# Kernel tuning notes

Hardware: AMD Instinct MI355X
Metric: run time of the kernel (lower is better)

The kernel has to match this reference:

```python
import jax, jax.numpy as jnp
import numpy as np

N, E, F_IN, HID, EDIM = 20000, 320000, 16, 64, 1


def _add_self_loops(src, dst, eattr, n):
    # PyG add_self_loops with fill_value='mean': self-loop edge_attr = mean of
    # incoming edge_attr per destination node (0 if no incoming edges).
    deg = jax.ops.segment_sum(jnp.ones_like(eattr[:, 0]), dst, num_segments=n)
    mean_attr = jax.ops.segment_sum(eattr, dst, num_segments=n) / jnp.maximum(deg, 1.0)[:, None]
    loop = jnp.arange(n)
    return (jnp.concatenate([src, loop]), jnp.concatenate([dst, loop]),
            jnp.concatenate([eattr, mean_attr], axis=0))


def _gat_layer(x, src, dst, eattr, W, a_src, a_dst, We, a_e, b, heads, out_ch, n):
    # shared linear for src/dst (PyG GATConv with int in_channels)
    h = (x @ W).reshape(n, heads, out_ch)                      # [N,H,C]
    al_s = jnp.einsum('nhc,hc->nh', h, a_src)                  # [N,H]
    al_d = jnp.einsum('nhc,hc->nh', h, a_dst)
    ef = (eattr @ We).reshape(-1, heads, out_ch)               # [E,H,C]
    al_e = jnp.einsum('ehc,hc->eh', ef, a_e)                   # [E,H]
    alpha = jax.nn.leaky_relu(al_s[src] + al_d[dst] + al_e, 0.2)
    # segment softmax over destination node
    m = jax.ops.segment_max(alpha, dst, num_segments=n)
    m = jnp.where(jnp.isfinite(m), m, 0.0)
    ex = jnp.exp(alpha - m[dst])
    den = jax.ops.segment_sum(ex, dst, num_segments=n)
    coef = ex / (den[dst] + 1e-16)                             # [E,H]
    out = jax.ops.segment_sum(h[src] * coef[:, :, None], dst, num_segments=n)
    return out.reshape(n, heads * out_ch) + b


def setup_inputs() -> dict:
    key = jax.random.key(0)
    ks = jax.random.split(key, 24)
    s = 0.1
    inp = {
        'x': jax.random.normal(ks[0], (N, F_IN), jnp.float32),
        'edge_index': jax.random.randint(ks[1], (2, E), 0, N, jnp.int64),
        'edge_attr': jax.random.uniform(ks[2], (E, EDIM), jnp.float32),
        # layer 0: heads=4, in=16, out=64
        'W0': jax.random.normal(ks[3], (F_IN, 4 * HID), jnp.float32) * s,
        'as0': jax.random.normal(ks[4], (4, HID), jnp.float32) * s,
        'ad0': jax.random.normal(ks[5], (4, HID), jnp.float32) * s,
        'We0': jax.random.normal(ks[6], (EDIM, 4 * HID), jnp.float32) * s,
        'ae0': jax.random.normal(ks[7], (4, HID), jnp.float32) * s,
        'b0': jnp.zeros((4 * HID,), jnp.float32),
        # layer 1: heads=4, in=256, out=64
        'W1': jax.random.normal(ks[8], (4 * HID, 4 * HID), jnp.float32) * s,
        'as1': jax.random.normal(ks[9], (4, HID), jnp.float32) * s,
        'ad1': jax.random.normal(ks[10], (4, HID), jnp.float32) * s,
        'We1': jax.random.normal(ks[11], (EDIM, 4 * HID), jnp.float32) * s,
        'ae1': jax.random.normal(ks[12], (4, HID), jnp.float32) * s,
        'b1': jnp.zeros((4 * HID,), jnp.float32),
        # layer 2: heads=1, in=256, out=64
        'W2': jax.random.normal(ks[13], (4 * HID, HID), jnp.float32) * s,
        'as2': jax.random.normal(ks[14], (1, HID), jnp.float32) * s,
        'ad2': jax.random.normal(ks[15], (1, HID), jnp.float32) * s,
        'We2': jax.random.normal(ks[16], (EDIM, HID), jnp.float32) * s,
        'ae2': jax.random.normal(ks[17], (1, HID), jnp.float32) * s,
        'b2': jnp.zeros((HID,), jnp.float32),
        'ln_g': jnp.ones((HID,), jnp.float32),
        'ln_b': jnp.zeros((HID,), jnp.float32),
    }
    return inp


def reference(x, edge_index, edge_attr,
              W0, as0, ad0, We0, ae0, b0,
              W1, as1, ad1, We1, ae1, b1,
              W2, as2, ad2, We2, ae2, b2,
              ln_g, ln_b):
    n = x.shape[0]
    src, dst, eattr = _add_self_loops(edge_index[0], edge_index[1], edge_attr, n)
    h = _gat_layer(x, src, dst, eattr, W0, as0, ad0, We0, ae0, b0, 4, HID, n)
    h = jax.nn.elu(h)  # dropout is identity in eval
    h = _gat_layer(h, src, dst, eattr, W1, as1, ad1, We1, ae1, b1, 4, HID, n)
    h = jax.nn.elu(h)
    h = _gat_layer(h, src, dst, eattr, W2, as2, ad2, We2, ae2, b2, 1, HID, n)
    mu = jnp.mean(h, axis=-1, keepdims=True)
    var = jnp.mean((h - mu) ** 2, axis=-1, keepdims=True)
    return (h - mu) / jnp.sqrt(var + 1e-5) * ln_g + ln_b
```

## Files before the change

### kernel.cpp

```cpp
#include <hip/hip_runtime.h>
#include <hip/hip_bf16.h>
#include <math.h>


typedef __attribute__((ext_vector_type(8))) short short8;
typedef __attribute__((ext_vector_type(4))) float float4v;

#define CAP 64

__device__ __forceinline__ float wave_sum(float v) {
#pragma unroll
  for (int off = 32; off > 0; off >>= 1) v += __shfl_xor(v, off, 64);
  return v;
}

__device__ __forceinline__ unsigned short f2bf(float v) {
  unsigned u = __float_as_uint(v);
  unsigned r = u + 0x7fff + ((u >> 16) & 1);
  return (unsigned short)(r >> 16);
}

__device__ __forceinline__ float bf2f(unsigned short u) {
  return __uint_as_float(((unsigned)u) << 16);
}

__device__ __forceinline__ float sel4(float a, float b, float c, float d, int i) {
  return (i == 0) ? a : (i == 1) ? b : (i == 2) ? c : d;
}

__global__ __launch_bounds__(256) void k1_kernel(
    const float* __restrict__ x, const int* __restrict__ srcv, const int* __restrict__ dstv,
    const float* __restrict__ eattr,
    const float* __restrict__ W0, const float* __restrict__ as0, const float* __restrict__ ad0,
    const float* __restrict__ We0, const float* __restrict__ ae0,
    const float* __restrict__ W1, const float* __restrict__ as1, const float* __restrict__ ad1,
    const float* __restrict__ We1, const float* __restrict__ ae1,
    const float* __restrict__ W2, const float* __restrict__ as2, const float* __restrict__ ad2,
    const float* __restrict__ We2, const float* __restrict__ ae2,
    unsigned short* __restrict__ Wf1, unsigned short* __restrict__ Wf2,
    float* __restrict__ wedot, float* __restrict__ al0s, float* __restrict__ al0d,
    int* __restrict__ deg, int2* __restrict__ ebuf,
    int N, int E, int gD) {
  int b = blockIdx.x;
  int tid = threadIdx.x;
  if (b < 272) {
    int idx = b * 256 + tid;
    int j = idx & 7, lane = (idx >> 3) & 63, ks = (idx >> 9) & 7, nt = idx >> 12;
    int k = ks * 32 + (lane >> 4) * 8 + j;
    int col = lane & 15;
    float v = 0.f;
    if (nt < 16) {
      v = W1[(size_t)k * 256 + nt * 16 + col];
    } else if (col < 4) {
      for (int c = 0; c < 64; c++) v = fmaf(W1[(size_t)k * 256 + col * 64 + c], as1[col * 64 + c], v);
    } else if (col < 8) {
      int h = col - 4;
      for (int c = 0; c < 64; c++) v = fmaf(W1[(size_t)k * 256 + h * 64 + c], ad1[h * 64 + c], v);
    }
    Wf1[idx] = f2bf(v);
  } else if (b < 352) {
    int idx = (b - 272) * 256 + tid;
    int j = idx & 7, lane = (idx >> 3) & 63, ks = (idx >> 9) & 7, nt = idx >> 12;
    int k = ks * 32 + (lane >> 4) * 8 + j;
    int col = lane & 15;
    float v = 0.f;
    if (nt < 4) {
      v = W2[(size_t)k * 64 + nt * 16 + col];
    } else if (col < 1) {
      for (int c = 0; c < 64; c++) v = fmaf(W2[(size_t)k * 64 + c], as2[c], v);
    } else if (col < 2) {
      for (int c = 0; c < 64; c++) v = fmaf(W2[(size_t)k * 64 + c], ad2[c], v);
    }
    Wf2[idx] = f2bf(v);
  } else if (b == 352) {
    if (tid >= 64) return;
    int c = tid;
    for (int h = 0; h < 4; h++) {
      float v = wave_sum(We0[h * 64 + c] * ae0[h * 64 + c]);
      if (c == 0) wedot[h] = v;
    }
    for (int h = 0; h < 4; h++) {
      float v = wave_sum(We1[h * 64 + c] * ae1[h * 64 + c]);
      if (c == 0) wedot[4 + h] = v;
    }
    float v = wave_sum(We2[c] * ae2[c]);
    if (c == 0) wedot[8] = v;
  } else if (b < 353 + gD) {
    __shared__ float va[128];
    if (tid < 128) {
      int k = tid >> 3, col = tid & 7;
      float v = 0.f;
      if (col < 4) {
        for (int c = 0; c < 64; c++) v = fmaf(W0[(size_t)k * 256 + col * 64 + c], as0[col * 64 + c], v);
      } else {
        int h = col - 4;
        for (int c = 0; c < 64; c++) v = fmaf(W0[(size_t)k * 256 + h * 64 + c], ad0[h * 64 + c], v);
      }
      va[tid] = v;
    }
    __syncthreads();
    int node = (b - 353) * 256 + tid;
    if (node >= N) return;
    const float4* xr = (const float4*)(x + (size_t)node * 16);
    float4 xv[4];
#pragma unroll
    for (int q = 0; q < 4; q++) xv[q] = xr[q];
    float al[8];
#pragma unroll
    for (int j = 0; j < 8; j++) al[j] = 0.f;
#pragma unroll
    for (int k = 0; k < 16; k++) {
      float xk = ((const float*)xv)[k];
#pragma unroll
      for (int j = 0; j < 8; j++) al[j] = fmaf(xk, va[k * 8 + j], al[j]);
    }
    ((float4*)al0s)[node] = make_float4(al[0], al[1], al[2], al[3]);
    ((float4*)al0d)[node] = make_float4(al[4], al[5], al[6], al[7]);
  } else {
    int e = (b - 353 - gD) * 256 + tid;
    if (e >= E) return;
    int d = dstv[e];
    int s = srcv[e];
    float ea = eattr[e];
    int pos = atomicAdd(&deg[d], 1);
    if (pos < CAP) ebuf[(size_t)d * CAP + pos] = make_int2(s, __float_as_int(ea));
  }
}

__global__ __launch_bounds__(1024) void fused0_kernel(
    const int* __restrict__ deg, const int2* __restrict__ ebuf,
    const float* __restrict__ al0s, const float* __restrict__ al0d,
    const float* __restrict__ wedot,
    const float* __restrict__ x, const float* __restrict__ W0,
    const float* __restrict__ b0, const unsigned short* __restrict__ Wf1,
    unsigned short* __restrict__ buf256, float* __restrict__ al1s,
    float* __restrict__ al1d, int n) {
  __shared__ unsigned short hrow[16][264];
  __shared__ float w0lds[4096];
  int tile = blockIdx.x;
  int wv = threadIdx.x >> 6;
  int lane = threadIdx.x & 63;
  int es = lane >> 4;
  int c = lane & 15;
  int le = lane >> 2;
  int lh = lane & 3;

  ((float4*)w0lds)[threadIdx.x] = ((const float4*)W0)[threadIdx.x];
  __syncthreads();

  int r = wv;
  int node = tile * 16 + r;
  if (node < n) {
    int dg = deg[node];
    int cnt = dg < CAP ? dg : CAP;
    float xself = x[(size_t)node * 16 + c];
    float4 as4s = ((const float4*)al0s)[node];
    float4 ald4 = ((const float4*)al0d)[node];
    float aldP = sel4(ald4.x, ald4.y, ald4.z, ald4.w, lh);
    float wd0 = wedot[0], wd1 = wedot[1], wd2 = wedot[2], wd3 = wedot[3];
    float wdP = sel4(wd0, wd1, wd2, wd3, lh);

    float Z[4] = {0.f, 0.f, 0.f, 0.f};
    float denP = 0.f;
    float easumP = 0.f;

    for (int i = 0; i < cnt; i += 16) {
      int slot = i + le;
      bool av = slot < cnt;
      int2 re = ebuf[(size_t)node * CAP + slot];
      int srcE = av ? re.x : 0;
      float ev = av ? __int_as_float(re.y) : 0.f;
      int srcK[4];
      float xvK[4];
#pragma unroll
      for (int k = 0; k < 4; k++) srcK[k] = __shfl(srcE, (k * 4 + es) * 4, 64);
#pragma unroll
      for (int k = 0; k < 4; k++) xvK[k] = x[(size_t)srcK[k] * 16 + c];
      float a = al0s[(size_t)srcE * 4 + lh] + aldP + ev * wdP;
      a = fmaxf(a, 0.2f * a);
      a = fminf(a, 30.f);
      float wE = av ? __expf(a) : 0.f;
      denP += wE;
      easumP += (lh == 0) ? ev : 0.f;
#pragma unroll
      for (int k = 0; k < 4; k++) {
        int e4 = (k * 4 + es) * 4;
        float w0v = __shfl(wE, e4 + 0, 64);
        float w1v = __shfl(wE, e4 + 1, 64);
        float w2v = __shfl(wE, e4 + 2, 64);
        float w3v = __shfl(wE, e4 + 3, 64);
        Z[0] = fmaf(w0v, xvK[k], Z[0]);
        Z[1] = fmaf(w1v, xvK[k], Z[1]);
        Z[2] = fmaf(w2v, xvK[k], Z[2]);
        Z[3] = fmaf(w3v, xvK[k], Z[3]);
      }
    }

#pragma unroll
    for (int h = 0; h < 4; h++) {
      Z[h] += __shfl_xor(Z[h], 16, 64);
      Z[h] += __shfl_xor(Z[h], 32, 64);
    }
    denP += __shfl_xor(denP, 4, 64);
    denP += __shfl_xor(denP, 8, 64);
    denP += __shfl_xor(denP, 16, 64);
    denP += __shfl_xor(denP, 32, 64);
    float easum = wave_sum(easumP);

    float dsel = __shfl(denP, es, 64);
    float evs = easum / fmaxf((float)dg, 1.f);
    float as_e = sel4(as4s.x, as4s.y, as4s.z, as4s.w, es);
    float ald_e = sel4(ald4.x, ald4.y, ald4.z, ald4.w, es);
    float wd_e = sel4(wd0, wd1, wd2, wd3, es);
    float aS = as_e + ald_e + evs * wd_e;
    aS = fmaxf(aS, 0.2f * aS);
    aS = fminf(aS, 30.f);
    float wvs = __expf(aS);
    dsel += wvs;
    float zsel = sel4(Z[0], Z[1], Z[2], Z[3], es) + wvs * xself;
    float zn = zsel / (dsel + 1e-16f);

    float zc[16];
    int basel = lane & 48;
#pragma unroll
    for (int cc = 0; cc < 16; cc++) zc[cc] = __shfl(zn, basel + cc, 64);
    float o[4];
    float4 b4 = ((const float4*)b0)[lane];
#pragma unroll
    for (int jj = 0; jj < 4; jj++) o[jj] = ((const float*)&b4)[jj];
#pragma unroll
    for (int cc = 0; cc < 16; cc++) {
      float4 w0r = *(const float4*)&w0lds[cc * 256 + lane * 4];
#pragma unroll
      for (int jj = 0; jj < 4; jj++) o[jj] = fmaf(zc[cc], ((const float*)&w0r)[jj], o[jj]);
    }
    ushort4 o4;
    float ox = o[0] > 0.f ? o[0] : expm1f(o[0]);
    float oy = o[1] > 0.f ? o[1] : expm1f(o[1]);
    float oz = o[2] > 0.f ? o[2] : expm1f(o[2]);
    float ow = o[3] > 0.f ? o[3] : expm1f(o[3]);
    o4.x = f2bf(ox);
    o4.y = f2bf(oy);
    o4.z = f2bf(oz);
    o4.w = f2bf(ow);
    *(ushort4*)&hrow[r][lane * 4] = o4;
  } else {
    *(ushort4*)&hrow[r][lane * 4] = make_ushort4(0, 0, 0, 0);
  }
  __syncthreads();

  int m = lane & 15, q = lane >> 4;
  int row0 = tile * 16;
  short8 afrag[8];
#pragma unroll
  for (int ks = 0; ks < 8; ks++) afrag[ks] = *(short8*)&hrow[m][ks * 32 + q * 8];

  const short8* wf = (const short8*)Wf1;
  for (int nt = wv; nt < 17; nt += 16) {
    const short8* bl = wf + (size_t)nt * 8 * 64 + lane;
    short8 bf[8];
#pragma unroll
    for (int ks = 0; ks < 8; ks++) bf[ks] = bl[ks * 64];
    float4v acc = {0.f, 0.f, 0.f, 0.f};
#pragma unroll
    for (int ks = 0; ks < 8; ks++)
      acc = __builtin_amdgcn_mfma_f32_16x16x32_bf16(afrag[ks], bf[ks], acc, 0, 0, 0);
    if (nt < 16) {
      int col = nt * 16 + m;
#pragma unroll
      for (int reg = 0; reg < 4; reg++) {
        int rr = row0 + q * 4 + reg;
        if (rr < n) buf256[(size_t)rr * 256 + col] = f2bf(acc[reg]);
      }
    } else {
#pragma unroll
      for (int reg = 0; reg < 4; reg++) {
        int rr = row0 + q * 4 + reg;
        if (rr < n) {
          if (m < 4) al1s[(size_t)rr * 4 + m] = acc[reg];
          else if (m < 8) al1d[(size_t)rr * 4 + (m - 4)] = acc[reg];
        }
      }
    }
  }
}

__global__ __launch_bounds__(1024) void fused1_kernel(
    const int* __restrict__ deg, const int2* __restrict__ ebuf,
    const float* __restrict__ al1s, const float* __restrict__ al1d,
    const float* __restrict__ wedot,
    const unsigned short* __restrict__ buf256, const float* __restrict__ b1,
    const unsigned short* __restrict__ Wf2, unsigned short* __restrict__ buf64,
    float* __restrict__ al2s, float* __restrict__ al2d, int n) {
  __shared__ unsigned short hrow[16][264];
  int tile = blockIdx.x;
  int wv = threadIdx.x >> 6;
  int lane = threadIdx.x & 63;
  int half = lane >> 5;
  int l = lane & 31;
  int h4 = l >> 3;
  int le = lane >> 2;
  int lh = lane & 3;
  int eA0 = half ? 1 : 0;
  int eB0 = half ? 3 : 2;

  int r = wv;
  int node = tile * 16 + r;
  if (node < n) {
    int dg = deg[node];
    int cnt = dg < CAP ? dg : CAP;
    float aldh = al1d[(size_t)node * 4 + h4];
    float alsh = al1s[(size_t)node * 4 + h4];
    float wdh = wedot[4 + h4];
    float aldP = al1d[(size_t)node * 4 + lh];
    float wdP = wedot[4 + lh];
    short8 rowS = ((const short8*)(buf256 + (size_t)node * 256))[l];

    float acc[8];
#pragma unroll
    for (int j = 0; j < 8; j++) acc[j] = 0.f;
    float denP = 0.f;
    float easumP = 0.f;

    for (int i = 0; i < cnt; i += 16) {
      int slot = i + le;
      bool av = slot < cnt;
      int2 re = ebuf[(size_t)node * CAP + slot];
      int srcE = av ? re.x : 0;
      float ev = av ? __int_as_float(re.y) : 0.f;
      int srcA[4], srcB[4];
#pragma unroll
      for (int k = 0; k < 4; k++) {
        srcA[k] = __shfl(srcE, (k * 4 + eA0) * 4, 64);
        srcB[k] = __shfl(srcE, (k * 4 + eB0) * 4, 64);
      }
      short8 rowA[4], rowB[4];
#pragma unroll
      for (int k = 0; k < 4; k++) {
        rowA[k] = ((const short8*)(buf256 + (size_t)srcA[k] * 256))[l];
        rowB[k] = ((const short8*)(buf256 + (size_t)srcB[k] * 256))[l];
      }
      float a = al1s[(size_t)srcE * 4 + lh] + aldP + ev * wdP;
      a = fmaxf(a, 0.2f * a);
      a = fminf(a, 30.f);
      float wE = av ? __expf(a) : 0.f;
      denP += wE;
      easumP += (lh == 0) ? ev : 0.f;
#pragma unroll
      for (int k = 0; k < 4; k++) {
        float wA = __shfl(wE, (k * 4 + eA0) * 4 + h4, 64);
        float wB = __shfl(wE, (k * 4 + eB0) * 4 + h4, 64);
        const unsigned short* pa = (const unsigned short*)&rowA[k];
        const unsigned short* pb = (const unsigned short*)&rowB[k];
#pragma unroll
        for (int j = 0; j < 8; j++) acc[j] = fmaf(wA, bf2f(pa[j]), acc[j]);
#pragma unroll
        for (int j = 0; j < 8; j++) acc[j] = fmaf(wB, bf2f(pb[j]), acc[j]);
      }
    }

#pragma unroll
    for (int j = 0; j < 8; j++) acc[j] += __shfl_xor(acc[j], 32, 64);
    denP += __shfl_xor(denP, 4, 64);
    denP += __shfl_xor(denP, 8, 64);
    denP += __shfl_xor(denP, 16, 64);
    denP += __shfl_xor(denP, 32, 64);
    float easum = wave_sum(easumP);
    float den = __shfl(denP, h4, 64);

    {
      float evs = easum / fmaxf((float)dg, 1.f);
      float a = alsh + aldh + evs * wdh;
      a = fmaxf(a, 0.2f * a);
      a = fminf(a, 30.f);
      float wvv = __expf(a);
      const unsigned short* ps = (const unsigned short*)&rowS;
      den += wvv;
#pragma unroll
      for (int j = 0; j < 8; j++) acc[j] = fmaf(wvv, bf2f(ps[j]), acc[j]);
    }

    if (half == 0) {
      float inv = 1.f / (den + 1e-16f);
      float4 bb0 = ((const float4*)b1)[l * 2];
      float4 bb1 = ((const float4*)b1)[l * 2 + 1];
      unsigned short o8[8];
#pragma unroll
      for (int j = 0; j < 8; j++) {
        float bjv = (j < 4) ? ((const float*)&bb0)[j] : ((const float*)&bb1)[j - 4];
        float o = acc[j] * inv + bjv;
        o = o > 0.f ? o : expm1f(o);
        o8[j] = f2bf(o);
      }
      *(short8*)&hrow[r][l * 8] = *(short8*)o8;
    }
  } else if (half == 0) {
    unsigned short z8[8] = {0, 0, 0, 0, 0, 0, 0, 0};
    *(short8*)&hrow[r][l * 8] = *(short8*)z8;
  }
  __syncthreads();

  int m = lane & 15, q = lane >> 4;
  int row0 = tile * 16;
  short8 afrag[8];
#pragma unroll
  for (int ks = 0; ks < 8; ks++) afrag[ks] = *(short8*)&hrow[m][ks * 32 + q * 8];

  const short8* wf = (const short8*)Wf2;
  for (int nt = wv; nt < 5; nt += 16) {
    const short8* bl = wf + (size_t)nt * 8 * 64 + lane;
    short8 bf[8];
#pragma unroll
    for (int ks = 0; ks < 8; ks++) bf[ks] = bl[ks * 64];
    float4v acc = {0.f, 0.f, 0.f, 0.f};
#pragma unroll
    for (int ks = 0; ks < 8; ks++)
      acc = __builtin_amdgcn_mfma_f32_16x16x32_bf16(afrag[ks], bf[ks], acc, 0, 0, 0);
    if (nt < 4) {
      int col = nt * 16 + m;
#pragma unroll
      for (int reg = 0; reg < 4; reg++) {
        int rr = row0 + q * 4 + reg;
        if (rr < n) buf64[(size_t)rr * 64 + col] = f2bf(acc[reg]);
      }
    } else {
#pragma unroll
      for (int reg = 0; reg < 4; reg++) {
        int rr = row0 + q * 4 + reg;
        if (rr < n) {
          if (m < 1) al2s[rr] = acc[reg];
          else if (m < 2) al2d[rr] = acc[reg];
        }
      }
    }
  }
}

__global__ __launch_bounds__(256) void agg_ln_kernel(
    const int* __restrict__ deg, const int2* __restrict__ ebuf,
    const float* __restrict__ al2s, const float* __restrict__ al2d,
    const float* __restrict__ wedot,
    const unsigned short* __restrict__ B, const float* __restrict__ bias,
    const float* __restrict__ ln_g, const float* __restrict__ ln_b,
    float* __restrict__ out, int n) {
  int wv = threadIdx.x >> 6;
  int node = blockIdx.x * 4 + wv;
  if (node >= n) return;
  int lane = threadIdx.x & 63;
  int q = lane >> 4;
  int l = lane & 15;
  int le = lane & 15;
  int dg = deg[node];
  int cnt = dg < CAP ? dg : CAP;
  float ald = al2d[node];
  float als = al2s[node];
  float wd = wedot[0];
  ushort4 bvS = ((const ushort4*)(B + (size_t)node * 64))[l];

  float4 acc = make_float4(0.f, 0.f, 0.f, 0.f);
  float denP = 0.f;
  float easumP = 0.f;

  for (int i = 0; i < cnt; i += 16) {
    int slot = i + le;
    bool av = slot < cnt;
    int2 re = ebuf[(size_t)node * CAP + slot];
    int srcE = av ? re.x : 0;
    float ev = av ? __int_as_float(re.y) : 0.f;
    int srcK[4];
#pragma unroll
    for (int k = 0; k < 4; k++) srcK[k] = __shfl(srcE, k * 4 + q, 64);
    ushort4 bvK[4];
#pragma unroll
    for (int k = 0; k < 4; k++) bvK[k] = ((const ushort4*)(B + (size_t)srcK[k] * 64))[l];
    float a = al2s[srcE] + ald + ev * wd;
    a = fmaxf(a, 0.2f * a);
    a = fminf(a, 30.f);
    float wE = av ? __expf(a) : 0.f;
    denP += wE;
    easumP += ev;
#pragma unroll
    for (int k = 0; k < 4; k++) {
      float w = __shfl(wE, k * 4 + q, 64);
      acc.x = fmaf(w, bf2f(bvK[k].x), acc.x);
      acc.y = fmaf(w, bf2f(bvK[k].y), acc.y);
      acc.z = fmaf(w, bf2f(bvK[k].z), acc.z);
      acc.w = fmaf(w, bf2f(bvK[k].w), acc.w);
    }
  }

  acc.x += __shfl_xor(acc.x, 32, 64);
  acc.y += __shfl_xor(acc.y, 32, 64);
  acc.z += __shfl_xor(acc.z, 32, 64);
  acc.w += __shfl_xor(acc.w, 32, 64);
  acc.x += __shfl_xor(acc.x, 16, 64);
  acc.y += __shfl_xor(acc.y, 16, 64);
  acc.z += __shfl_xor(acc.z, 16, 64);
  acc.w += __shfl_xor(acc.w, 16, 64);
  float den = wave_sum(denP) * 0.25f;
  float easum = wave_sum(easumP) * 0.25f;

  {
    float evs = easum / fmaxf((float)dg, 1.f);
    float a = als + ald + evs * wd;
    a = fmaxf(a, 0.2f * a);
    a = fminf(a, 30.f);
    float wv2 = __expf(a);
    den += wv2;
    acc.x = fmaf(wv2, bf2f(bvS.x), acc.x);
    acc.y = fmaf(wv2, bf2f(bvS.y), acc.y);
    acc.z = fmaf(wv2, bf2f(bvS.z), acc.z);
    acc.w = fmaf(wv2, bf2f(bvS.w), acc.w);
  }

  float inv = 1.f / (den + 1e-16f);
  float4 b4 = ((const float4*)bias)[l];
  float4 o;
  o.x = acc.x * inv + b4.x;
  o.y = acc.y * inv + b4.y;
  o.z = acc.z * inv + b4.z;
  o.w = acc.w * inv + b4.w;
  float s = (o.x + o.y) + (o.z + o.w);
#pragma unroll
  for (int off = 1; off < 16; off <<= 1) s += __shfl_xor(s, off, 64);
  float mu = s * (1.f / 64.f);
  float dx = o.x - mu, dy = o.y - mu, dz = o.z - mu, dw = o.w - mu;
  float v = (dx * dx + dy * dy) + (dz * dz + dw * dw);
#pragma unroll
  for (int off = 1; off < 16; off <<= 1) v += __shfl_xor(v, off, 64);
  float rs = rsqrtf(v * (1.f / 64.f) + 1e-5f);
  if (q == 0) {
    float4 g4 = ((const float4*)ln_g)[l];
    float4 lb4 = ((const float4*)ln_b)[l];
    float4 rr;
    rr.x = dx * rs * g4.x + lb4.x;
    rr.y = dy * rs * g4.y + lb4.y;
    rr.z = dz * rs * g4.z + lb4.z;
    rr.w = dw * rs * g4.w + lb4.w;
    ((float4*)(out + (size_t)node * 64))[l] = rr;
  }
}

extern "C" void kernel_launch(void* const* d_in, const int* in_sizes, int n_in,
                              void* d_out, int out_size, void* d_ws, size_t ws_size,
                              hipStream_t stream) {
  const float* x = (const float*)d_in[0];
  const int* ei = (const int*)d_in[1];
  const float* eattr = (const float*)d_in[2];
  const float* W0 = (const float*)d_in[3];
  const float* as0 = (const float*)d_in[4];
  const float* ad0 = (const float*)d_in[5];
  const float* We0 = (const float*)d_in[6];
  const float* ae0 = (const float*)d_in[7];
  const float* b0 = (const float*)d_in[8];
  const float* W1 = (const float*)d_in[9];
  const float* as1 = (const float*)d_in[10];
  const float* ad1 = (const float*)d_in[11];
  const float* We1 = (const float*)d_in[12];
  const float* ae1 = (const float*)d_in[13];
  const float* b1 = (const float*)d_in[14];
  const float* W2 = (const float*)d_in[15];
  const float* as2 = (const float*)d_in[16];
  const float* ad2 = (const float*)d_in[17];
  const float* We2 = (const float*)d_in[18];
  const float* ae2 = (const float*)d_in[19];
  const float* b2 = (const float*)d_in[20];
  const float* lng = (const float*)d_in[21];
  const float* lnb = (const float*)d_in[22];
  float* outp = (float*)d_out;

  const int N = in_sizes[0] / 16;
  const int E = in_sizes[1] / 2;
  const int* srcv = ei;
  const int* dstv = ei + E;

  char* w = (char*)d_ws;
  size_t off = 0;
  auto alloc = [&](size_t bytes) -> void* {
    void* p = w + off;
    off += (bytes + 255) & ~(size_t)255;
    return p;
  };
  int* deg = (int*)alloc((size_t)N * 4);
  size_t zero_bytes = off;
  int2* ebuf = (int2*)alloc(((size_t)N * CAP + 16) * 8);
  float* wedot = (float*)alloc(16 * 4);
  float* al0s = (float*)alloc((size_t)N * 4 * 4);
  float* al0d = (float*)alloc((size_t)N * 4 * 4);
  float* al1s = (float*)alloc((size_t)N * 4 * 4);
  float* al1d = (float*)alloc((size_t)N * 4 * 4);
  float* al2s = (float*)alloc((size_t)N * 4);
  float* al2d = (float*)alloc((size_t)N * 4);
  unsigned short* Wf1 = (unsigned short*)alloc((size_t)17 * 4096 * 2);
  unsigned short* Wf2 = (unsigned short*)alloc((size_t)5 * 4096 * 2);
  unsigned short* buf256 = (unsigned short*)alloc((size_t)N * 256 * 2);
  unsigned short* buf64 = (unsigned short*)alloc((size_t)N * 64 * 2);
  (void)ws_size;

  hipMemsetAsync(d_ws, 0, zero_bytes, stream);

  int gE = (E + 255) / 256;
  int gD = (N + 255) / 256;

  k1_kernel<<<353 + gD + gE, 256, 0, stream>>>(
      x, srcv, dstv, eattr, W0, as0, ad0, We0, ae0, W1, as1, ad1, We1, ae1,
      W2, as2, ad2, We2, ae2, Wf1, Wf2, wedot, al0s, al0d, deg, ebuf, N, E, gD);

  int gT = (N + 15) / 16;
  int gNode4 = (N + 3) / 4;

  fused0_kernel<<<gT, 1024, 0, stream>>>(deg, ebuf, al0s, al0d, wedot, x, W0, b0,
                                         Wf1, buf256, al1s, al1d, N);

  fused1_kernel<<<gT, 1024, 0, stream>>>(deg, ebuf, al1s, al1d, wedot, buf256, b1,
                                         Wf2, buf64, al2s, al2d, N);

  agg_ln_kernel<<<gNode4, 256, 0, stream>>>(deg, ebuf, al2s, al2d, wedot + 8,
                                            buf64, b2, lng, lnb, outp, N);
}
```

Before: 210.8 us.

## Split fused aggregate+GEMM kernels into separate aggregation and MFMA GEMM kernels

Each of the two fused 1024-thread aggregate-then-GEMM kernels becomes a 256-thread aggregation kernel (one wave per node) followed by a standalone templated MFMA GEMM kernel that reads bf16 rows from global memory. The intent is to drop the block-wide barrier and LDS staging, which left 16 waves per block idle while the GEMM ran on only a few of them, and to raise occupancy through launch_bounds with min-blocks hints. The cost is two extra kernel launches and a round trip of the 256-wide bf16 hidden activations through global memory. The buffers are renamed to two ping-pong arrays of N×256.

```diff
diff --git a/kernel.cpp b/kernel.cpp
--- a/kernel.cpp
+++ b/kernel.cpp
@@ -127,136 +127,147 @@
   }
 }
 
-__global__ __launch_bounds__(1024) void fused0_kernel(
+__global__ __launch_bounds__(256, 8) void agg0p_kernel(
     const int* __restrict__ deg, const int2* __restrict__ ebuf,
     const float* __restrict__ al0s, const float* __restrict__ al0d,
     const float* __restrict__ wedot,
     const float* __restrict__ x, const float* __restrict__ W0,
-    const float* __restrict__ b0, const unsigned short* __restrict__ Wf1,
-    unsigned short* __restrict__ buf256, float* __restrict__ al1s,
-    float* __restrict__ al1d, int n) {
-  __shared__ unsigned short hrow[16][264];
+    const float* __restrict__ b0, unsigned short* __restrict__ out, int n) {
   __shared__ float w0lds[4096];
-  int tile = blockIdx.x;
+#pragma unroll
+  for (int i = 0; i < 4; i++) {
+    int idx = i * 256 + threadIdx.x;
+    ((float4*)w0lds)[idx] = ((const float4*)W0)[idx];
+  }
+  __syncthreads();
+
   int wv = threadIdx.x >> 6;
+  int node = blockIdx.x * 4 + wv;
+  if (node >= n) return;
   int lane = threadIdx.x & 63;
   int es = lane >> 4;
   int c = lane & 15;
   int le = lane >> 2;
   int lh = lane & 3;
 
-  ((float4*)w0lds)[threadIdx.x] = ((const float4*)W0)[threadIdx.x];
-  __syncthreads();
-
-  int r = wv;
-  int node = tile * 16 + r;
-  if (node < n) {
-    int dg = deg[node];
-    int cnt = dg < CAP ? dg : CAP;
-    float xself = x[(size_t)node * 16 + c];
-    float4 as4s = ((const float4*)al0s)[node];
-    float4 ald4 = ((const float4*)al0d)[node];
-    float aldP = sel4(ald4.x, ald4.y, ald4.z, ald4.w, lh);
-    float wd0 = wedot[0], wd1 = wedot[1], wd2 = wedot[2], wd3 = wedot[3];
-    float wdP = sel4(wd0, wd1, wd2, wd3, lh);
-
-    float Z[4] = {0.f, 0.f, 0.f, 0.f};
-    float denP = 0.f;
-    float easumP = 0.f;
-
-    for (int i = 0; i < cnt; i += 16) {
-      int slot = i + le;
-      bool av = slot < cnt;
-      int2 re = ebuf[(size_t)node * CAP + slot];
-      int srcE = av ? re.x : 0;
-      float ev = av ? __int_as_float(re.y) : 0.f;
-      int srcK[4];
-      float xvK[4];
-#pragma unroll
-      for (int k = 0; k < 4; k++) srcK[k] = __shfl(srcE, (k * 4 + es) * 4, 64);
-#pragma unroll
-      for (int k = 0; k < 4; k++) xvK[k] = x[(size_t)srcK[k] * 16 + c];
-      float a = al0s[(size_t)srcE * 4 + lh] + aldP + ev * wdP;
-      a = fmaxf(a, 0.2f * a);
-      a = fminf(a, 30.f);
-      float wE = av ? __expf(a) : 0.f;
-      denP += wE;
-      easumP += (lh == 0) ? ev : 0.f;
-#pragma unroll
-      for (int k = 0; k < 4; k++) {
-        int e4 = (k * 4 + es) * 4;
-        float w0v = __shfl(wE, e4 + 0, 64);
-        float w1v = __shfl(wE, e4 + 1, 64);
-        float w2v = __shfl(wE, e4 + 2, 64);
-        float w3v = __shfl(wE, e4 + 3, 64);
-        Z[0] = fmaf(w0v, xvK[k], Z[0]);
-        Z[1] = fmaf(w1v, xvK[k], Z[1]);
-        Z[2] = fmaf(w2v, xvK[k], Z[2]);
-        Z[3] = fmaf(w3v, xvK[k], Z[3]);
-      }
-    }
-
-#pragma unroll
-    for (int h = 0; h < 4; h++) {
-      Z[h] += __shfl_xor(Z[h], 16, 64);
-      Z[h] += __shfl_xor(Z[h], 32, 64);
-    }
-    denP += __shfl_xor(denP, 4, 64);
-    denP += __shfl_xor(denP, 8, 64);
-    denP += __shfl_xor(denP, 16, 64);
-    denP += __shfl_xor(denP, 32, 64);
-    float easum = wave_sum(easumP);
-
-    float dsel = __shfl(denP, es, 64);
-    float evs = easum / fmaxf((float)dg, 1.f);
-    float as_e = sel4(as4s.x, as4s.y, as4s.z, as4s.w, es);
-    float ald_e = sel4(ald4.x, ald4.y, ald4.z, ald4.w, es);
-    float wd_e = sel4(wd0, wd1, wd2, wd3, es);
-    float aS = as_e + ald_e + evs * wd_e;
-    aS = fmaxf(aS, 0.2f * aS);
-    aS = fminf(aS, 30.f);
-    float wvs = __expf(aS);
-    dsel += wvs;
-    float zsel = sel4(Z[0], Z[1], Z[2], Z[3], es) + wvs * xself;
-    float zn = zsel / (dsel + 1e-16f);
-
-    float zc[16];
-    int basel = lane & 48;
-#pragma unroll
-    for (int cc = 0; cc < 16; cc++) zc[cc] = __shfl(zn, basel + cc, 64);
-    float o[4];
-    float4 b4 = ((const float4*)b0)[lane];
-#pragma unroll
-    for (int jj = 0; jj < 4; jj++) o[jj] = ((const float*)&b4)[jj];
-#pragma unroll
-    for (int cc = 0; cc < 16; cc++) {
-      float4 w0r = *(const float4*)&w0lds[cc * 256 + lane * 4];
-#pragma unroll
-      for (int jj = 0; jj < 4; jj++) o[jj] = fmaf(zc[cc], ((const float*)&w0r)[jj], o[jj]);
-    }
-    ushort4 o4;
-    float ox = o[0] > 0.f ? o[0] : expm1f(o[0]);
-    float oy = o[1] > 0.f ? o[1] : expm1f(o[1]);
-    float oz = o[2] > 0.f ? o[2] : expm1f(o[2]);
-    float ow = o[3] > 0.f ? o[3] : expm1f(o[3]);
-    o4.x = f2bf(ox);
-    o4.y = f2bf(oy);
-    o4.z = f2bf(oz);
-    o4.w = f2bf(ow);
-    *(ushort4*)&hrow[r][lane * 4] = o4;
+  int dg = deg[node];
+  int cnt = dg < CAP ? dg : CAP;
+  float xself = x[(size_t)node * 16 + c];
+  float4 as4s = ((const float4*)al0s)[node];
+  float4 ald4 = ((const float4*)al0d)[node];
+  float aldP = sel4(ald4.x, ald4.y, ald4.z, ald4.w, lh);
+  float wd0 = wedot[0], wd1 = wedot[1], wd2 = wedot[2], wd3 = wedot[3];
+  float wdP = sel4(wd0, wd1, wd2, wd3, lh);
+
+  float Z[4] = {0.f, 0.f, 0.f, 0.f};
+  float denP = 0.f;
+  float easumP = 0.f;
+
+  for (int i = 0; i < cnt; i += 16) {
+    int slot = i + le;
+    bool av = slot < cnt;
+    int2 re = ebuf[(size_t)node * CAP + slot];
+    int srcE = av ? re.x : 0;
+    float ev = av ? __int_as_float(re.y) : 0.f;
+    int srcK[4];
+    float xvK[4];
+#pragma unroll
+    for (int k = 0; k < 4; k++) srcK[k] = __shfl(srcE, (k * 4 + es) * 4, 64);
+#pragma unroll
+    for (int k = 0; k < 4; k++) xvK[k] = x[(size_t)srcK[k] * 16 + c];
+    float a = al0s[(size_t)srcE * 4 + lh] + aldP + ev * wdP;
+    a = fmaxf(a, 0.2f * a);
+    a = fminf(a, 30.f);
+    float wE = av ? __expf(a) : 0.f;
+    denP += wE;
+    easumP += (lh == 0) ? ev : 0.f;
+#pragma unroll
+    for (int k = 0; k < 4; k++) {
+      int e4 = (k * 4 + es) * 4;
+      float w0v = __shfl(wE, e4 + 0, 64);
+      float w1v = __shfl(wE, e4 + 1, 64);
+      float w2v = __shfl(wE, e4 + 2, 64);
+      float w3v = __shfl(wE, e4 + 3, 64);
+      Z[0] = fmaf(w0v, xvK[k], Z[0]);
+      Z[1] = fmaf(w1v, xvK[k], Z[1]);
+      Z[2] = fmaf(w2v, xvK[k], Z[2]);
+      Z[3] = fmaf(w3v, xvK[k], Z[3]);
+    }
+  }
+
+#pragma unroll
+  for (int h = 0; h < 4; h++) {
+    Z[h] += __shfl_xor(Z[h], 16, 64);
+    Z[h] += __shfl_xor(Z[h], 32, 64);
+  }
+  denP += __shfl_xor(denP, 4, 64);
+  denP += __shfl_xor(denP, 8, 64);
+  denP += __shfl_xor(denP, 16, 64);
+  denP += __shfl_xor(denP, 32, 64);
+  float easum = wave_sum(easumP);
+
+  float dsel = __shfl(denP, es, 64);
+  float evs = easum / fmaxf((float)dg, 1.f);
+  float as_e = sel4(as4s.x, as4s.y, as4s.z, as4s.w, es);
+  float ald_e = sel4(ald4.x, ald4.y, ald4.z, ald4.w, es);
+  float wd_e = sel4(wd0, wd1, wd2, wd3, es);
+  float aS = as_e + ald_e + evs * wd_e;
+  aS = fmaxf(aS, 0.2f * aS);
+  aS = fminf(aS, 30.f);
+  float wvs = __expf(aS);
+  dsel += wvs;
+  float zsel = sel4(Z[0], Z[1], Z[2], Z[3], es) + wvs * xself;
+  float zn = zsel / (dsel + 1e-16f);
+
+  float o[4];
+  float4 b4 = ((const float4*)b0)[lane];
+#pragma unroll
+  for (int jj = 0; jj < 4; jj++) o[jj] = ((const float*)&b4)[jj];
+  int basel = lane & 48;
+#pragma unroll
+  for (int cc = 0; cc < 16; cc++) {
+    float zc = __shfl(zn, basel + cc, 64);
+    float4 w0r = *(const float4*)&w0lds[cc * 256 + lane * 4];
+#pragma unroll
+    for (int jj = 0; jj < 4; jj++) o[jj] = fmaf(zc, ((const float*)&w0r)[jj], o[jj]);
+  }
+  ushort4 o4;
+  float ox = o[0] > 0.f ? o[0] : expm1f(o[0]);
+  float oy = o[1] > 0.f ? o[1] : expm1f(o[1]);
+  float oz = o[2] > 0.f ? o[2] : expm1f(o[2]);
+  float ow = o[3] > 0.f ? o[3] : expm1f(o[3]);
+  o4.x = f2bf(ox);
+  o4.y = f2bf(oy);
+  o4.z = f2bf(oz);
+  o4.w = f2bf(ow);
+  ((ushort4*)out)[(size_t)node * 64 + lane] = o4;
+}
+
+template <int M, int H>
+__global__ __launch_bounds__(256, 4) void gemm_kernel(
+    const unsigned short* __restrict__ Abf, const unsigned short* __restrict__ Wfrag,
+    unsigned short* __restrict__ out, float* __restrict__ al_s, float* __restrict__ al_d,
+    int n) {
+  int lane = threadIdx.x & 63;
+  int wv = threadIdx.x >> 6;
+  int row0 = blockIdx.x * 64 + wv * 16;
+  int m = lane & 15, q = lane >> 4;
+
+  short8 afrag[8];
+  int r = row0 + m;
+  if (r < n) {
+    const short8* arow = (const short8*)(Abf + (size_t)r * 256);
+#pragma unroll
+    for (int ks = 0; ks < 8; ks++) afrag[ks] = arow[ks * 4 + q];
   } else {
-    *(ushort4*)&hrow[r][lane * 4] = make_ushort4(0, 0, 0, 0);
-  }
-  __syncthreads();
-
-  int m = lane & 15, q = lane >> 4;
-  int row0 = tile * 16;
-  short8 afrag[8];
-#pragma unroll
-  for (int ks = 0; ks < 8; ks++) afrag[ks] = *(short8*)&hrow[m][ks * 32 + q * 8];
-
-  const short8* wf = (const short8*)Wf1;
-  for (int nt = wv; nt < 17; nt += 16) {
+#pragma unroll
+    for (int ks = 0; ks < 8; ks++) afrag[ks] = (short8)0;
+  }
+
+  const short8* wf = (const short8*)Wfrag;
+
+#pragma unroll 1
+  for (int nt = 0; nt < M / 16; nt++) {
     const short8* bl = wf + (size_t)nt * 8 * 64 + lane;
     short8 bf[8];
 #pragma unroll
@@ -265,36 +276,43 @@
 #pragma unroll
     for (int ks = 0; ks < 8; ks++)
       acc = __builtin_amdgcn_mfma_f32_16x16x32_bf16(afrag[ks], bf[ks], acc, 0, 0, 0);
-    if (nt < 16) {
-      int col = nt * 16 + m;
-#pragma unroll
-      for (int reg = 0; reg < 4; reg++) {
-        int rr = row0 + q * 4 + reg;
-        if (rr < n) buf256[(size_t)rr * 256 + col] = f2bf(acc[reg]);
+    int col = nt * 16 + m;
+#pragma unroll
+    for (int reg = 0; reg < 4; reg++) {
+      int rr = row0 + q * 4 + reg;
+      if (rr < n) out[(size_t)rr * M + col] = f2bf(acc[reg]);
+    }
+  }
+
+  {
+    const short8* bl = wf + (size_t)(M / 16) * 8 * 64 + lane;
+    short8 bf[8];
+#pragma unroll
+    for (int ks = 0; ks < 8; ks++) bf[ks] = bl[ks * 64];
+    float4v acc = {0.f, 0.f, 0.f, 0.f};
+#pragma unroll
+    for (int ks = 0; ks < 8; ks++)
+      acc = __builtin_amdgcn_mfma_f32_16x16x32_bf16(afrag[ks], bf[ks], acc, 0, 0, 0);
+#pragma unroll
+    for (int reg = 0; reg < 4; reg++) {
+      int rr = row0 + q * 4 + reg;
+      if (rr < n) {
+        if (m < H) al_s[(size_t)rr * H + m] = acc[reg];
+        else if (m < 2 * H) al_d[(size_t)rr * H + (m - H)] = acc[reg];
       }
-    } else {
-#pragma unroll
-      for (int reg = 0; reg < 4; reg++) {
-        int rr = row0 + q * 4 + reg;
-        if (rr < n) {
-          if (m < 4) al1s[(size_t)rr * 4 + m] = acc[reg];
-          else if (m < 8) al1d[(size_t)rr * 4 + (m - 4)] = acc[reg];
-        }
-      }
-    }
-  }
-}
-
-__global__ __launch_bounds__(1024) void fused1_kernel(
+    }
+  }
+}
+
+__global__ __launch_bounds__(256, 8) void agg4_kernel(
     const int* __restrict__ deg, const int2* __restrict__ ebuf,
     const float* __restrict__ al1s, const float* __restrict__ al1d,
     const float* __restrict__ wedot,
-    const unsigned short* __restrict__ buf256, const float* __restrict__ b1,
-    const unsigned short* __restrict__ Wf2, unsigned short* __restrict__ buf64,
-    float* __restrict__ al2s, float* __restrict__ al2d, int n) {
-  __shared__ unsigned short hrow[16][264];
-  int tile = blockIdx.x;
+    const unsigned short* __restrict__ B, const float* __restrict__ b1,
+    unsigned short* __restrict__ out, int n) {
   int wv = threadIdx.x >> 6;
+  int node = blockIdx.x * 4 + wv;
+  if (node >= n) return;
   int lane = threadIdx.x & 63;
   int half = lane >> 5;
   int l = lane & 31;
@@ -304,139 +322,96 @@
   int eA0 = half ? 1 : 0;
   int eB0 = half ? 3 : 2;
 
-  int r = wv;
-  int node = tile * 16 + r;
-  if (node < n) {
-    int dg = deg[node];
-    int cnt = dg < CAP ? dg : CAP;
-    float aldh = al1d[(size_t)node * 4 + h4];
-    float alsh = al1s[(size_t)node * 4 + h4];
-    float wdh = wedot[4 + h4];
-    float aldP = al1d[(size_t)node * 4 + lh];
-    float wdP = wedot[4 + lh];
-    short8 rowS = ((const short8*)(buf256 + (size_t)node * 256))[l];
-
-    float acc[8];
-#pragma unroll
-    for (int j = 0; j < 8; j++) acc[j] = 0.f;
-    float denP = 0.f;
-    float easumP = 0.f;
-
-    for (int i = 0; i < cnt; i += 16) {
-      int slot = i + le;
-      bool av = slot < cnt;
-      int2 re = ebuf[(size_t)node * CAP + slot];
-      int srcE = av ? re.x : 0;
-      float ev = av ? __int_as_float(re.y) : 0.f;
-      int srcA[4], srcB[4];
-#pragma unroll
-      for (int k = 0; k < 4; k++) {
-        srcA[k] = __shfl(srcE, (k * 4 + eA0) * 4, 64);
-        srcB[k] = __shfl(srcE, (k * 4 + eB0) * 4, 64);
-      }
-      short8 rowA[4], rowB[4];
-#pragma unroll
-      for (int k = 0; k < 4; k++) {
-        rowA[k] = ((const short8*)(buf256 + (size_t)srcA[k] * 256))[l];
-        rowB[k] = ((const short8*)(buf256 + (size_t)srcB[k] * 256))[l];
-      }
-      float a = al1s[(size_t)srcE * 4 + lh] + aldP + ev * wdP;
-      a = fmaxf(a, 0.2f * a);
-      a = fminf(a, 30.f);
-      float wE = av ? __expf(a) : 0.f;
-      denP += wE;
-      easumP += (lh == 0) ? ev : 0.f;
-#pragma unroll
-      for (int k = 0; k < 4; k++) {
-        float wA = __shfl(wE, (k * 4 + eA0) * 4 + h4, 64);
-        float wB = __shfl(wE, (k * 4 + eB0) * 4 + h4, 64);
-        const unsigned short* pa = (const unsigned short*)&rowA[k];
-        const unsigned short* pb = (const unsigned short*)&rowB[k];
-#pragma unroll
-        for (int j = 0; j < 8; j++) acc[j] = fmaf(wA, bf2f(pa[j]), acc[j]);
-#pragma unroll
-        for (int j = 0; j < 8; j++) acc[j] = fmaf(wB, bf2f(pb[j]), acc[j]);
-      }
-    }
-
-#pragma unroll
-    for (int j = 0; j < 8; j++) acc[j] += __shfl_xor(acc[j], 32, 64);
-    denP += __shfl_xor(denP, 4, 64);
-    denP += __shfl_xor(denP, 8, 64);
-    denP += __shfl_xor(denP, 16, 64);
-    denP += __shfl_xor(denP, 32, 64);
-    float easum = wave_sum(easumP);
-    float den = __shfl(denP, h4, 64);
-
-    {
-      float evs = easum / fmaxf((float)dg, 1.f);
-      float a = alsh + aldh + evs * wdh;
-      a = fmaxf(a, 0.2f * a);
-      a = fminf(a, 30.f);
-      float wvv = __expf(a);
-      const unsigned short* ps = (const unsigned short*)&rowS;
-      den += wvv;
-#pragma unroll
-      for (int j = 0; j < 8; j++) acc[j] = fmaf(wvv, bf2f(ps[j]), acc[j]);
-    }
-
-    if (half == 0) {
-      float inv = 1.f / (den + 1e-16f);
-      float4 bb0 = ((const float4*)b1)[l * 2];
-      float4 bb1 = ((const float4*)b1)[l * 2 + 1];
-      unsigned short o8[8];
-#pragma unroll
-      for (int j = 0; j < 8; j++) {
-        float bjv = (j < 4) ? ((const float*)&bb0)[j] : ((const float*)&bb1)[j - 4];
-        float o = acc[j] * inv + bjv;
-        o = o > 0.f ? o : expm1f(o);
-        o8[j] = f2bf(o);
-      }
-      *(short8*)&hrow[r][l * 8] = *(short8*)o8;
-    }
-  } else if (half == 0) {
-    unsigned short z8[8] = {0, 0, 0, 0, 0, 0, 0, 0};
-    *(short8*)&hrow[r][l * 8] = *(short8*)z8;
-  }
-  __syncthreads();
-
-  int m = lane & 15, q = lane >> 4;
-  int row0 = tile * 16;
-  short8 afrag[8];
-#pragma unroll
-  for (int ks = 0; ks < 8; ks++) afrag[ks] = *(short8*)&hrow[m][ks * 32 + q * 8];
-
-  const short8* wf = (const short8*)Wf2;
-  for (int nt = wv; nt < 5; nt += 16) {
-    const short8* bl = wf + (size_t)nt * 8 * 64 + lane;
-    short8 bf[8];
-#pragma unroll
-    for (int ks = 0; ks < 8; ks++) bf[ks] = bl[ks * 64];
-    float4v acc = {0.f, 0.f, 0.f, 0.f};
-#pragma unroll
-    for (int ks = 0; ks < 8; ks++)
-      acc = __builtin_amdgcn_mfma_f32_16x16x32_bf16(afrag[ks], bf[ks], acc, 0, 0, 0);
-    if (nt < 4) {
-      int col = nt * 16 + m;
-#pragma unroll
-      for (int reg = 0; reg < 4; reg++) {
-        int rr = row0 + q * 4 + reg;
-        if (rr < n) buf64[(size_t)rr * 64 + col] = f2bf(acc[reg]);
-      }
-    } else {
-#pragma unroll
-      for (int reg = 0; reg < 4; reg++) {
-        int rr = row0 + q * 4 + reg;
-        if (rr < n) {
-          if (m < 1) al2s[rr] = acc[reg];
-          else if (m < 2) al2d[rr] = acc[reg];
-        }
-      }
-    }
-  }
-}
-
-__global__ __launch_bounds__(256) void agg_ln_kernel(
+  int dg = deg[node];
+  int cnt = dg < CAP ? dg : CAP;
+  float aldh = al1d[(size_t)node * 4 + h4];
+  float alsh = al1s[(size_t)node * 4 + h4];
+  float wdh = wedot[4 + h4];
+  float aldP = al1d[(size_t)node * 4 + lh];
+  float wdP = wedot[4 + lh];
+  short8 rowS = ((const short8*)(B + (size_t)node * 256))[l];
+
+  float acc[8];
+#pragma unroll
+  for (int j = 0; j < 8; j++) acc[j] = 0.f;
+  float denP = 0.f;
+  float easumP = 0.f;
+
+  for (int i = 0; i < cnt; i += 16) {
+    int slot = i + le;
+    bool av = slot < cnt;
+    int2 re = ebuf[(size_t)node * CAP + slot];
+    int srcE = av ? re.x : 0;
+    float ev = av ? __int_as_float(re.y) : 0.f;
+    int srcA[4], srcB[4];
+#pragma unroll
+    for (int k = 0; k < 4; k++) {
+      srcA[k] = __shfl(srcE, (k * 4 + eA0) * 4, 64);
+      srcB[k] = __shfl(srcE, (k * 4 + eB0) * 4, 64);
+    }
+    short8 rowA[4], rowB[4];
+#pragma unroll
+    for (int k = 0; k < 4; k++) {
+      rowA[k] = ((const short8*)(B + (size_t)srcA[k] * 256))[l];
+      rowB[k] = ((const short8*)(B + (size_t)srcB[k] * 256))[l];
+    }
+    float a = al1s[(size_t)srcE * 4 + lh] + aldP + ev * wdP;
+    a = fmaxf(a, 0.2f * a);
+    a = fminf(a, 30.f);
+    float wE = av ? __expf(a) : 0.f;
+    denP += wE;
+    easumP += (lh == 0) ? ev : 0.f;
+#pragma unroll
+    for (int k = 0; k < 4; k++) {
+      float wA = __shfl(wE, (k * 4 + eA0) * 4 + h4, 64);
+      float wB = __shfl(wE, (k * 4 + eB0) * 4 + h4, 64);
+      const unsigned short* pa = (const unsigned short*)&rowA[k];
+      const unsigned short* pb = (const unsigned short*)&rowB[k];
+#pragma unroll
+      for (int j = 0; j < 8; j++) acc[j] = fmaf(wA, bf2f(pa[j]), acc[j]);
+#pragma unroll
+      for (int j = 0; j < 8; j++) acc[j] = fmaf(wB, bf2f(pb[j]), acc[j]);
+    }
+  }
+
+#pragma unroll
+  for (int j = 0; j < 8; j++) acc[j] += __shfl_xor(acc[j], 32, 64);
+  denP += __shfl_xor(denP, 4, 64);
+  denP += __shfl_xor(denP, 8, 64);
+  denP += __shfl_xor(denP, 16, 64);
+  denP += __shfl_xor(denP, 32, 64);
+  float easum = wave_sum(easumP);
+  float den = __shfl(denP, h4, 64);
+
+  {
+    float evs = easum / fmaxf((float)dg, 1.f);
+    float a = alsh + aldh + evs * wdh;
+    a = fmaxf(a, 0.2f * a);
+    a = fminf(a, 30.f);
+    float wvv = __expf(a);
+    const unsigned short* ps = (const unsigned short*)&rowS;
+    den += wvv;
+#pragma unroll
+    for (int j = 0; j < 8; j++) acc[j] = fmaf(wvv, bf2f(ps[j]), acc[j]);
+  }
+
+  if (half == 0) {
+    float inv = 1.f / (den + 1e-16f);
+    float4 bb0 = ((const float4*)b1)[l * 2];
+    float4 bb1 = ((const float4*)b1)[l * 2 + 1];
+    unsigned short o8[8];
+#pragma unroll
+    for (int j = 0; j < 8; j++) {
+      float bjv = (j < 4) ? ((const float*)&bb0)[j] : ((const float*)&bb1)[j - 4];
+      float o = acc[j] * inv + bjv;
+      o = o > 0.f ? o : expm1f(o);
+      o8[j] = f2bf(o);
+    }
+    ((short8*)(out + (size_t)node * 256))[l] = *(short8*)o8;
+  }
+}
+
+__global__ __launch_bounds__(256, 8) void agg_ln_kernel(
     const int* __restrict__ deg, const int2* __restrict__ ebuf,
     const float* __restrict__ al2s, const float* __restrict__ al2d,
     const float* __restrict__ wedot,
@@ -593,8 +568,8 @@
   float* al2d = (float*)alloc((size_t)N * 4);
   unsigned short* Wf1 = (unsigned short*)alloc((size_t)17 * 4096 * 2);
   unsigned short* Wf2 = (unsigned short*)alloc((size_t)5 * 4096 * 2);
-  unsigned short* buf256 = (unsigned short*)alloc((size_t)N * 256 * 2);
-  unsigned short* buf64 = (unsigned short*)alloc((size_t)N * 64 * 2);
+  unsigned short* bufA = (unsigned short*)alloc((size_t)N * 256 * 2);
+  unsigned short* bufB = (unsigned short*)alloc((size_t)N * 256 * 2);
   (void)ws_size;
 
   hipMemsetAsync(d_ws, 0, zero_bytes, stream);
@@ -606,15 +581,19 @@
       x, srcv, dstv, eattr, W0, as0, ad0, We0, ae0, W1, as1, ad1, We1, ae1,
       W2, as2, ad2, We2, ae2, Wf1, Wf2, wedot, al0s, al0d, deg, ebuf, N, E, gD);
 
-  int gT = (N + 15) / 16;
   int gNode4 = (N + 3) / 4;
-
-  fused0_kernel<<<gT, 1024, 0, stream>>>(deg, ebuf, al0s, al0d, wedot, x, W0, b0,
-                                         Wf1, buf256, al1s, al1d, N);
-
-  fused1_kernel<<<gT, 1024, 0, stream>>>(deg, ebuf, al1s, al1d, wedot, buf256, b1,
-                                         Wf2, buf64, al2s, al2d, N);
+  int gRow64 = (N + 63) / 64;
+
+  agg0p_kernel<<<gNode4, 256, 0, stream>>>(deg, ebuf, al0s, al0d, wedot, x, W0, b0,
+                                           bufA, N);
+
+  gemm_kernel<256, 4><<<gRow64, 256, 0, stream>>>(bufA, Wf1, bufB, al1s, al1d, N);
+
+  agg4_kernel<<<gNode4, 256, 0, stream>>>(deg, ebuf, al1s, al1d, wedot, bufB, b1,
+                                          bufA, N);
+
+  gemm_kernel<64, 1><<<gRow64, 256, 0, stream>>>(bufA, Wf2, bufB, al2s, al2d, N);
 
   agg_ln_kernel<<<gNode4, 256, 0, stream>>>(deg, ebuf, al2s, al2d, wedot + 8,
-                                            buf64, b2, lng, lnb, outp, N);
-}
+                                            bufB, b2, lng, lnb, outp, N);
+}
```

Measured after the change: 297.3 us. +41.0%, slower.
